# Performance work log

Hardware: AMD Instinct MI355X
Metric: run time of the kernel (lower is better)

The kernel has to match this reference:

```python
import jax, jax.numpy as jnp
import numpy as np

DIM = 512
HEADS = 8
DIM_HEAD = 64
DIM_INNER = HEADS * DIM_HEAD
FRAC_GRAD = 0.5
SCALE = DIM_HEAD ** -0.5
EPS_CUMPROD = 1e-10
EPS_INV = 1e-8


def setup_inputs() -> dict:
    key = jax.random.key(0)
    ks = jax.random.split(key, 8)
    b, n = 2, 2048
    x = jax.random.normal(ks[0], (b, n, DIM), dtype=jnp.float32)
    gamma = jnp.ones((DIM,), dtype=jnp.float32)
    w_qkv = jax.random.normal(ks[1], (DIM, 3 * DIM_INNER), dtype=jnp.float32) * 0.02
    b_qkv = jnp.zeros((3 * DIM_INNER,), dtype=jnp.float32)
    # to_a: torch init is zeros weight + bias 10; use small random weight and
    # moderate bias so the decay gate is non-trivial for correctness testing
    w_a = jax.random.normal(ks[2], (DIM, DIM_INNER), dtype=jnp.float32) * 0.02
    b_a = jnp.full((DIM_INNER,), 2.0, dtype=jnp.float32)
    w_out = jax.random.normal(ks[3], (DIM_INNER, DIM), dtype=jnp.float32) * 0.02
    b_out = jnp.zeros((DIM,), dtype=jnp.float32)
    return {"x": x, "gamma": gamma, "w_qkv": w_qkv, "b_qkv": b_qkv,
            "w_a": w_a, "b_a": b_a, "w_out": w_out, "b_out": b_out}


def _rms_norm(x, gamma):
    # F.normalize(x, dim=-1) * sqrt(dim) * gamma
    nrm = jnp.linalg.norm(x, axis=-1, keepdims=True)
    return x / jnp.maximum(nrm, 1e-12) * (DIM ** 0.5) * gamma


def _safe_cumprod(t, axis):
    t = jnp.clip(t, EPS_CUMPROD, 1.0)
    return jnp.exp(jnp.cumsum(jnp.log(t), axis=axis))


def reference(x, gamma, w_qkv, b_qkv, w_a, b_a, w_out, b_out):
    b, n, _ = x.shape
    x = _rms_norm(x, gamma)

    qkv = x @ w_qkv + b_qkv  # [b, n, 3*h*d]
    qkv = qkv.reshape(b, n, 3, HEADS, DIM_HEAD).transpose(2, 0, 3, 1, 4)  # [3,b,h,n,d]
    q, k, v = qkv[0], qkv[1], qkv[2]
    q = q * SCALE

    # data-dependent relative-position decay gate
    a = (x @ w_a + b_a).reshape(b, n, HEADS, DIM_HEAD).transpose(0, 2, 1, 3)  # [b,h,n,d]
    a = a * FRAC_GRAD + jax.lax.stop_gradient(a) * (1.0 - FRAC_GRAD)
    a = jax.nn.sigmoid(a)
    a_cum = _safe_cumprod(a, axis=-2)
    a_cum_inv = 1.0 / jnp.maximum(a_cum, EPS_INV)

    q = q * a_cum
    k = k * a_cum_inv

    sim = jnp.einsum('bhid,bhjd->bhij', q, k)
    causal_mask = jnp.triu(jnp.ones((n, n), dtype=bool), k=1)
    attn = jnp.where(causal_mask, 0.0, sim)  # no softmax in decay branch

    out = jnp.einsum('bhij,bhjd->bhid', attn, v)  # [b,h,n,d]
    out = out.transpose(0, 2, 1, 3).reshape(b, n, DIM_INNER)
    return out @ w_out + b_out
```

## Files before the change

kernel.cpp:

```cpp
#include <hip/hip_runtime.h>
#include <hip/hip_cooperative_groups.h>


namespace cg = cooperative_groups;

using s8v   = __attribute__((ext_vector_type(8))) short;
using f32x4 = __attribute__((ext_vector_type(4))) float;

__device__ __forceinline__ unsigned short f2b(float f) {
  unsigned int u = __builtin_bit_cast(unsigned int, f);
  u += 0x7FFFu + ((u >> 16) & 1u);
  return (unsigned short)(u >> 16);
}
__device__ __forceinline__ float b2f(unsigned short b) {
  unsigned int u = ((unsigned int)b) << 16;
  return __builtin_bit_cast(float, u);
}
__device__ __forceinline__ f32x4 mfma16(s8v a, s8v b, f32x4 c) {
  return __builtin_amdgcn_mfma_f32_16x16x32_bf16(a, b, c, 0, 0, 0);
}
__device__ __forceinline__ void gload16(const void* g, void* l) {
  __builtin_amdgcn_global_load_lds(
      (const __attribute__((address_space(1))) void*)g,
      (__attribute__((address_space(3))) void*)l, 16, 0, 0);
}

__device__ __forceinline__ void st_prep(int u, int tid, char* arena,
    const float* __restrict__ x, const float* __restrict__ gamma,
    short* __restrict__ xnb,
    const float* __restrict__ w_qkv, const float* __restrict__ w_a,
    const float* __restrict__ w_out,
    short* __restrict__ wT, short* __restrict__ woT) {
  int lane = tid & 63, wave = tid >> 6;
  if (u < 1024) {
    int row = u * 4 + wave;
    const float4* xp = reinterpret_cast<const float4*>(x + (size_t)row * 512 + lane * 8);
    float4 v0 = xp[0], v1 = xp[1];
    float ss = v0.x*v0.x + v0.y*v0.y + v0.z*v0.z + v0.w*v0.w
             + v1.x*v1.x + v1.y*v1.y + v1.z*v1.z + v1.w*v1.w;
#pragma unroll
    for (int off = 32; off > 0; off >>= 1) ss += __shfl_xor(ss, off, 64);
    float s = 22.627416997969522f / fmaxf(sqrtf(ss), 1e-12f);
    const float* g = gamma + lane * 8;
    float vals[8] = {v0.x, v0.y, v0.z, v0.w, v1.x, v1.y, v1.z, v1.w};
    s8v o;
#pragma unroll
    for (int j = 0; j < 8; ++j) o[j] = (short)f2b(vals[j] * s * g[j]);
    *reinterpret_cast<s8v*>(xnb + (size_t)row * 512 + lane * 8) = o;
  } else {
    float (*t)[33] = reinterpret_cast<float (*)[33]>(arena);
    int id = u - 1024;
    int bx = id % 80, k0 = (id / 80) * 32;
    const float* src; short* dst; int N, n0;
    if (bx < 48)      { src = w_qkv; dst = wT;                      N = 1536; n0 = bx * 32; }
    else if (bx < 64) { src = w_a;   dst = wT + (size_t)1536 * 512; N = 512;  n0 = (bx - 48) * 32; }
    else              { src = w_out; dst = woT;                     N = 512;  n0 = (bx - 64) * 32; }
    int tx = tid & 31, ty = tid >> 5;
    __syncthreads();
#pragma unroll
    for (int i = 0; i < 4; ++i)
      t[ty + 8 * i][tx] = src[(size_t)(k0 + ty + 8 * i) * N + n0 + tx];
    __syncthreads();
#pragma unroll
    for (int i = 0; i < 4; ++i)
      dst[(size_t)(n0 + ty + 8 * i) * 512 + k0 + tx] = (short)f2b(t[tx][ty + 8 * i]);
  }
}

template <int BM, int BN, int FM, int FN>
__device__ __forceinline__ void gemm_core(const short* __restrict__ A,
                                          const short* __restrict__ Bm,
                                          char* LA, char* LB,
                                          int m0, int n0, int tid,
                                          f32x4 (&acc)[FM][FN]) {
  const int lane = tid & 63, wave = tid >> 6;
  const int wr = (wave >> 1) * (BM / 2), wc = (wave & 1) * (BN / 2);
#pragma unroll 1
  for (int t = 0; t < 8; ++t) {
    const int k0 = t * 64;
#pragma unroll
    for (int r = 0; r < BM / 32; ++r) {
      int o = r * 4096 + tid * 16;
      int row = o >> 7;
      int ce = (((o & 127) ^ ((row & 7) << 4)) >> 1);
      gload16(A + (size_t)(m0 + row) * 512 + k0 + ce, LA + o);
    }
#pragma unroll
    for (int r = 0; r < BN / 32; ++r) {
      int o = r * 4096 + tid * 16;
      int row = o >> 7;
      int ce = (((o & 127) ^ ((row & 7) << 4)) >> 1);
      gload16(Bm + (size_t)(n0 + row) * 512 + k0 + ce, LB + o);
    }
    __syncthreads();
#pragma unroll
    for (int kk = 0; kk < 2; ++kk) {
      s8v af[FM], bf[FN];
#pragma unroll
      for (int m = 0; m < FM; ++m) {
        int row = wr + m * 16 + (lane & 15);
        int ad = ((row << 7) + kk * 64 + ((lane >> 4) << 4)) ^ ((row & 7) << 4);
        af[m] = *reinterpret_cast<const s8v*>(LA + ad);
      }
#pragma unroll
      for (int n = 0; n < FN; ++n) {
        int row = wc + n * 16 + (lane & 15);
        int ad = ((row << 7) + kk * 64 + ((lane >> 4) << 4)) ^ ((row & 7) << 4);
        bf[n] = *reinterpret_cast<const s8v*>(LB + ad);
      }
#pragma unroll
      for (int m = 0; m < FM; ++m)
#pragma unroll
        for (int n = 0; n < FN; ++n)
          acc[m][n] = mfma16(af[m], bf[n], acc[m][n]);
    }
    if (t + 1 < 8) __syncthreads();
  }
}

__device__ __forceinline__ void st_gemm0(int vid, int tid, char* arena,
    const short* __restrict__ xnb, const short* __restrict__ wT,
    short* __restrict__ qkvb, const float* __restrict__ b_qkv,
    const float* __restrict__ b_a, float* __restrict__ araw,
    float* __restrict__ csum) {
  const int lane = tid & 63, wave = tid >> 6;
  int xcd = vid & 7, rq = vid >> 3;
  int bx = rq & 15, by = xcd * 4 + (rq >> 4);
  int m0 = by * 128, n0 = bx * 128;
  f32x4 acc[4][4] = {};
  gemm_core<128, 128, 4, 4>(xnb, wT, arena, arena + 16384, m0, n0, tid, acc);
  int wr = (wave >> 1) * 64, wc = (wave & 1) * 64;
  if (n0 < 1536) {
#pragma unroll
    for (int m = 0; m < 4; ++m)
#pragma unroll
      for (int n = 0; n < 4; ++n)
#pragma unroll
        for (int r = 0; r < 4; ++r) {
          int row = m0 + wr + m * 16 + ((lane >> 4) << 2) + r;
          int col = n0 + wc + n * 16 + (lane & 15);
          float v = acc[m][n][r] + b_qkv[col];
          int w = col >> 9, h = (col >> 6) & 7, d = col & 63;
          int b = row >> 11, nn = row & 2047;
          qkvb[((((size_t)(w * 2 + b)) * 8 + h) * 2048 + nn) * 64 + d] = (short)f2b(v);
        }
  } else {
    float cs[4] = {};
    int b = m0 >> 11;
#pragma unroll
    for (int m = 0; m < 4; ++m)
#pragma unroll
      for (int n = 0; n < 4; ++n)
#pragma unroll
        for (int r = 0; r < 4; ++r) {
          int row = m0 + wr + m * 16 + ((lane >> 4) << 2) + r;
          int gc = n0 + wc + n * 16 + (lane & 15) - 1536;
          int h = gc >> 6, d = gc & 63, nn = row & 2047;
          float xv = acc[m][n][r] + b_a[gc];
          araw[((size_t)(b * 8 + h) * 2048 + nn) * 64 + d] = xv;
          float a = 1.f / (1.f + expf(-xv));
          a = fminf(fmaxf(a, 1e-10f), 1.f);
          cs[n] += logf(a);
        }
#pragma unroll
    for (int n = 0; n < 4; ++n) {
      cs[n] += __shfl_xor(cs[n], 16, 64);
      cs[n] += __shfl_xor(cs[n], 32, 64);
    }
    int nsel = lane >> 4;
    float v = (nsel == 0) ? cs[0] : (nsel == 1) ? cs[1] : (nsel == 2) ? cs[2] : cs[3];
    int col = wc + nsel * 16 + (lane & 15);
    int gc = n0 + col - 1536;
    int h = gc >> 6, d = gc & 63;
    int chunkg = ((m0 & 2047) >> 6) + (wave >> 1);
    csum[(((size_t)(b * 8 + h)) * 32 + chunkg) * 64 + d] = v;
  }
}

__device__ __forceinline__ void st_scan2(int vid, int tid, char* arena,
    const short* __restrict__ qkvb, const float* __restrict__ araw,
    const float* __restrict__ csum, short* __restrict__ q2,
    short* __restrict__ k2, short* __restrict__ vT, short* __restrict__ Sbuf) {
  int chunk = vid & 31, bh = vid >> 5;
  int lane = tid & 63, wave = tid >> 6, d = lane;
  short (*kL)[64] = reinterpret_cast<short (*)[64]>(arena);
  short (*vL)[64] = reinterpret_cast<short (*)[64]>(arena + 8192);
  char* kT  = arena + 16384;
  char* vTl = arena + 24576;
  float (*wsum)[64] = reinterpret_cast<float (*)[64]>(arena + 16384);
  float pre = 0.f;
  for (int c = 0; c < chunk; ++c) pre += csum[((size_t)bh * 32 + c) * 64 + d];
  const float* ap = araw + ((size_t)bh * 2048 + chunk * 64 + wave * 16) * 64 + d;
  float la[16]; float run = 0.f;
#pragma unroll
  for (int rr = 0; rr < 16; ++rr) {
    float xv = ap[rr * 64];
    float a = 1.f / (1.f + expf(-xv));
    a = fminf(fmaxf(a, 1e-10f), 1.f);
    run += logf(a);
    la[rr] = run;
  }
  wsum[wave][d] = run;
  __syncthreads();
#pragma unroll
  for (int w = 0; w < 3; ++w) if (w < wave) pre += wsum[w][d];
  const size_t WS = (size_t)2 * 8 * 2048 * 64;
  size_t base = ((size_t)bh * 2048 + chunk * 64 + wave * 16) * 64 + d;
#pragma unroll 4
  for (int rr = 0; rr < 16; ++rr) {
    int r = wave * 16 + rr;
    float g = expf(pre + la[rr]);
    float gi = 1.f / fmaxf(g, 1e-8f);
    float qv = b2f((unsigned short)qkvb[base + rr * 64]);
    float kv = b2f((unsigned short)qkvb[base + WS + rr * 64]);
    short vb = qkvb[base + 2 * WS + rr * 64];
    q2[base + rr * 64] = (short)f2b(qv * 0.125f * g);
    unsigned short kb = f2b(kv * gi);
    k2[base + rr * 64] = (short)kb;
    kL[r][d] = (short)kb;
    vL[r][d] = vb;
  }
  __syncthreads();
  short* vTrow = vT + ((size_t)bh * 64 + d) * 2048 + chunk * 64;
#pragma unroll
  for (int gg = 0; gg < 2; ++gg) {
    int g8 = wave + gg * 4;
    s8v pk, pv;
#pragma unroll
    for (int j = 0; j < 8; ++j) { pk[j] = kL[g8 * 8 + j][d]; pv[j] = vL[g8 * 8 + j][d]; }
    *reinterpret_cast<s8v*>(vTrow + g8 * 8) = pv;
    int ad = ((d << 7) + g8 * 16) ^ ((d & 7) << 4);
    *reinterpret_cast<s8v*>(kT  + ad) = pk;
    *reinterpret_cast<s8v*>(vTl + ad) = pv;
  }
  __syncthreads();
  f32x4 acc[4] = {};
#pragma unroll
  for (int kk = 0; kk < 2; ++kk) {
    int arow = wave * 16 + (lane & 15);
    int aad = ((arow << 7) + kk * 64 + ((lane >> 4) << 4)) ^ ((arow & 7) << 4);
    s8v av = *reinterpret_cast<const s8v*>(vTl + aad);
#pragma unroll
    for (int n = 0; n < 4; ++n) {
      int brow = n * 16 + (lane & 15);
      int bad = ((brow << 7) + kk * 64 + ((lane >> 4) << 4)) ^ ((brow & 7) << 4);
      acc[n] = mfma16(av, *reinterpret_cast<const s8v*>(kT + bad), acc[n]);
    }
  }
  short* Sp = Sbuf + ((size_t)bh * 32 + chunk) * 4096;
#pragma unroll
  for (int n = 0; n < 4; ++n)
#pragma unroll
    for (int r = 0; r < 4; ++r)
      Sp[(wave * 16 + ((lane >> 4) << 2) + r) * 64 + n * 16 + (lane & 15)] = (short)f2b(acc[n][r]);
}

__device__ __forceinline__ void st_sprefix(int vid, int tid,
    const short* __restrict__ Sbuf, short* __restrict__ Spre) {
  int bh = vid >> 4;
  int e = ((vid & 15) << 8) + tid;
  size_t base = (size_t)bh * 32 * 4096 + e;
  float acc = 0.f;
  for (int c = 0; c < 32; ++c) {
    Spre[base + (size_t)c * 4096] = (short)f2b(acc);
    acc += b2f((unsigned short)Sbuf[base + (size_t)c * 4096]);
  }
}

__device__ __forceinline__ void st_attnk(int vid, int tid, char* arena,
    const short* __restrict__ q2, const short* __restrict__ k2,
    const short* __restrict__ vT, const short* __restrict__ Spre,
    short* __restrict__ aout) {
  int chunk = vid & 31, bh = vid >> 5;
  int lane = tid & 63, wave = tid >> 6;
  char* LQ = arena;
  char* LK = arena + 8192;
  char* LV = arena + 16384;
  char* LS = arena + 24576;
#pragma unroll
  for (int rr = 0; rr < 2; ++rr) {
    int o = rr * 4096 + tid * 16;
    int row = o >> 7;
    int ce = (((o & 127) ^ ((row & 7) << 4)) >> 1);
    gload16(q2   + ((size_t)bh * 2048 + chunk * 64 + row) * 64 + ce, LQ + o);
    gload16(k2   + ((size_t)bh * 2048 + chunk * 64 + row) * 64 + ce, LK + o);
    gload16(vT   + ((size_t)bh * 64 + row) * 2048 + chunk * 64 + ce, LV + o);
    gload16(Spre + (((size_t)bh * 32 + chunk) * 64 + row) * 64 + ce, LS + o);
  }
  __syncthreads();
  f32x4 accS[4] = {}, accO[4] = {};
#pragma unroll
  for (int kk = 0; kk < 2; ++kk) {
    int arow = wave * 16 + (lane & 15);
    int aad = ((arow << 7) + kk * 64 + ((lane >> 4) << 4)) ^ ((arow & 7) << 4);
    s8v aq = *reinterpret_cast<const s8v*>(LQ + aad);
#pragma unroll
    for (int n = 0; n < 4; ++n) {
      int brow = n * 16 + (lane & 15);
      int bad = ((brow << 7) + kk * 64 + ((lane >> 4) << 4)) ^ ((brow & 7) << 4);
      accS[n] = mfma16(aq, *reinterpret_cast<const s8v*>(LK + bad), accS[n]);
      accO[n] = mfma16(aq, *reinterpret_cast<const s8v*>(LS + bad), accO[n]);
    }
  }
  __syncthreads();
#pragma unroll
  for (int n = 0; n < 4; ++n)
#pragma unroll
    for (int r = 0; r < 4; ++r) {
      int i = wave * 16 + ((lane >> 4) << 2) + r;
      int j = n * 16 + (lane & 15);
      float v = (j <= i) ? accS[n][r] : 0.f;
      int ad = ((i << 7) + (j << 1)) ^ ((i & 7) << 4);
      *reinterpret_cast<short*>(LQ + ad) = (short)f2b(v);
    }
  __syncthreads();
#pragma unroll
  for (int kk = 0; kk < 2; ++kk) {
    int arow = wave * 16 + (lane & 15);
    int aad = ((arow << 7) + kk * 64 + ((lane >> 4) << 4)) ^ ((arow & 7) << 4);
    s8v ap = *reinterpret_cast<const s8v*>(LQ + aad);
#pragma unroll
    for (int n = 0; n < 4; ++n) {
      int brow = n * 16 + (lane & 15);
      int bad = ((brow << 7) + kk * 64 + ((lane >> 4) << 4)) ^ ((brow & 7) << 4);
      accO[n] = mfma16(ap, *reinterpret_cast<const s8v*>(LV + bad), accO[n]);
    }
  }
  int b = bh >> 3, h = bh & 7;
#pragma unroll
  for (int n = 0; n < 4; ++n)
#pragma unroll
    for (int r = 0; r < 4; ++r) {
      int i = wave * 16 + ((lane >> 4) << 2) + r;
      int col = h * 64 + n * 16 + (lane & 15);
      size_t row = (size_t)b * 2048 + chunk * 64 + i;
      aout[row * 512 + col] = (short)f2b(accO[n][r]);
    }
}

__device__ __forceinline__ void st_gemm1(int vid, int tid, char* arena,
    const short* __restrict__ aout, const short* __restrict__ woT,
    float* __restrict__ out, const float* __restrict__ b_out) {
  const int lane = tid & 63, wave = tid >> 6;
  int xcd = vid & 7, rq = vid >> 3;
  int bx = rq & 7, by = xcd * 8 + (rq >> 3);
  int m0 = by * 64, n0 = bx * 64;
  f32x4 acc[2][2] = {};
  gemm_core<64, 64, 2, 2>(aout, woT, arena, arena + 8192, m0, n0, tid, acc);
  int wr = (wave >> 1) * 32, wc = (wave & 1) * 32;
#pragma unroll
  for (int m = 0; m < 2; ++m)
#pragma unroll
    for (int n = 0; n < 2; ++n)
#pragma unroll
      for (int r = 0; r < 4; ++r) {
        int row = m0 + wr + m * 16 + ((lane >> 4) << 2) + r;
        int col = n0 + wc + n * 16 + (lane & 15);
        out[(size_t)row * 512 + col] = acc[m][n][r] + b_out[col];
      }
}

__global__ __launch_bounds__(256, 2) void mega_k(
    const float* __restrict__ x, const float* __restrict__ gamma,
    const float* __restrict__ w_qkv, const float* __restrict__ b_qkv,
    const float* __restrict__ w_a, const float* __restrict__ b_a,
    const float* __restrict__ w_out, const float* __restrict__ b_out,
    float* __restrict__ out,
    short* __restrict__ xnb, short* __restrict__ wT, short* __restrict__ woT,
    short* __restrict__ qkvb, float* __restrict__ araw, float* __restrict__ csum,
    short* __restrict__ q2, short* __restrict__ k2, short* __restrict__ vT,
    short* __restrict__ Sbuf, short* __restrict__ Spre, short* __restrict__ aout) {
  __shared__ __align__(16) char arena[32768];
  cg::grid_group grid = cg::this_grid();
  const int bid = blockIdx.x, tid = threadIdx.x;

  for (int u = bid; u < 2304; u += 512)
    st_prep(u, tid, arena, x, gamma, xnb, w_qkv, w_a, w_out, wT, woT);
  __threadfence(); grid.sync();

  st_gemm0(bid, tid, arena, xnb, wT, qkvb, b_qkv, b_a, araw, csum);
  __threadfence(); grid.sync();

  st_scan2(bid, tid, arena, qkvb, araw, csum, q2, k2, vT, Sbuf);
  __threadfence(); grid.sync();

  if (bid < 256) st_sprefix(bid, tid, Sbuf, Spre);
  __threadfence(); grid.sync();

  st_attnk(bid, tid, arena, q2, k2, vT, Spre, aout);
  __threadfence(); grid.sync();

  st_gemm1(bid, tid, arena, aout, woT, out, b_out);
}

__global__ __launch_bounds__(256) void prep_k(const float* x, const float* gamma,
    short* xnb, const float* w_qkv, const float* w_a, const float* w_out,
    short* wT, short* woT) {
  __shared__ __align__(16) char arena[4224];
  st_prep(blockIdx.x, threadIdx.x, arena, x, gamma, xnb, w_qkv, w_a, w_out, wT, woT);
}
__global__ __launch_bounds__(256) void gemm0_k(const short* xnb, const short* wT,
    short* qkvb, const float* b_qkv, const float* b_a, float* araw, float* csum) {
  __shared__ __align__(16) char arena[32768];
  st_gemm0(blockIdx.x, threadIdx.x, arena, xnb, wT, qkvb, b_qkv, b_a, araw, csum);
}
__global__ __launch_bounds__(256) void scan2_k(const short* qkvb, const float* araw,
    const float* csum, short* q2, short* k2, short* vT, short* Sbuf) {
  __shared__ __align__(16) char arena[32768];
  st_scan2(blockIdx.x, threadIdx.x, arena, qkvb, araw, csum, q2, k2, vT, Sbuf);
}
__global__ __launch_bounds__(256) void sprefix_k(const short* Sbuf, short* Spre) {
  st_sprefix(blockIdx.x, threadIdx.x, Sbuf, Spre);
}
__global__ __launch_bounds__(256) void attnk_k(const short* q2, const short* k2,
    const short* vT, const short* Spre, short* aout) {
  __shared__ __align__(16) char arena[32768];
  st_attnk(blockIdx.x, threadIdx.x, arena, q2, k2, vT, Spre, aout);
}
__global__ __launch_bounds__(256) void gemm1_k(const short* aout, const short* woT,
    float* out, const float* b_out) {
  __shared__ __align__(16) char arena[16384];
  st_gemm1(blockIdx.x, threadIdx.x, arena, aout, woT, out, b_out);
}

extern "C" void kernel_launch(void* const* d_in, const int* in_sizes, int n_in,
                              void* d_out, int out_size, void* d_ws, size_t ws_size,
                              hipStream_t stream) {
  const float* x     = (const float*)d_in[0];
  const float* gamma = (const float*)d_in[1];
  const float* w_qkv = (const float*)d_in[2];
  const float* b_qkv = (const float*)d_in[3];
  const float* w_a   = (const float*)d_in[4];
  const float* b_a   = (const float*)d_in[5];
  const float* w_out = (const float*)d_in[6];
  const float* b_out = (const float*)d_in[7];
  float* out = (float*)d_out;
  char* ws = (char*)d_ws;

  const size_t MB = 1u << 20;
  short* xnb  = (short*)(ws);
  short* wT   = (short*)(ws + 4  * MB);
  short* woT  = (short*)(ws + 6  * MB);
  short* qkvb = (short*)(ws + 7  * MB);
  float* araw = (float*)(ws + 19 * MB);
  float* csum = (float*)(ws + 27 * MB);
  short* q2   = (short*)(ws + 28 * MB);
  short* k2   = (short*)(ws + 32 * MB);
  short* vT   = (short*)(ws + 36 * MB);
  short* Sbuf = (short*)(ws + 40 * MB);
  short* Spre = (short*)(ws + 44 * MB);
  short* aout = (short*)(ws + 48 * MB);

  int dev = 0; (void)hipGetDevice(&dev);
  int coop = 0;
  (void)hipDeviceGetAttribute(&coop, hipDeviceAttributeCooperativeLaunch, dev);
  int nb = 0;
  (void)hipOccupancyMaxActiveBlocksPerMultiprocessor(&nb, mega_k, 256, 0);

  hipError_t err = hipErrorUnknown;
  if (coop && nb >= 2) {
    void* args[] = {&x, &gamma, &w_qkv, &b_qkv, &w_a, &b_a, &w_out, &b_out,
                    &out, &xnb, &wT, &woT, &qkvb, &araw, &csum,
                    &q2, &k2, &vT, &Sbuf, &Spre, &aout};
    err = hipLaunchCooperativeKernel((void*)mega_k, dim3(512), dim3(256), args, 0, stream);
  }
  if (err != hipSuccess) {
    prep_k   <<<2304, 256, 0, stream>>>(x, gamma, xnb, w_qkv, w_a, w_out, wT, woT);
    gemm0_k  <<<512,  256, 0, stream>>>(xnb, wT, qkvb, b_qkv, b_a, araw, csum);
    scan2_k  <<<512,  256, 0, stream>>>(qkvb, araw, csum, q2, k2, vT, Sbuf);
    sprefix_k<<<256,  256, 0, stream>>>(Sbuf, Spre);
    attnk_k  <<<512,  256, 0, stream>>>(q2, k2, vT, Spre, aout);
    gemm1_k  <<<512,  256, 0, stream>>>(aout, woT, out, b_out);
  }
}
```

Baseline: 70.98 us.

## Keep q/k/v chunk tiles in LDS across grid syncs in cooperative megakernel

```diff
diff --git a/kernel.cpp b/kernel.cpp
--- a/kernel.cpp
+++ b/kernel.cpp
@@ -368,11 +368,11 @@
     float* __restrict__ out,
     short* __restrict__ xnb, short* __restrict__ wT, short* __restrict__ woT,
     short* __restrict__ qkvb, float* __restrict__ araw, float* __restrict__ csum,
-    short* __restrict__ q2, short* __restrict__ k2, short* __restrict__ vT,
     short* __restrict__ Sbuf, short* __restrict__ Spre, short* __restrict__ aout) {
   __shared__ __align__(16) char arena[32768];
   cg::grid_group grid = cg::this_grid();
   const int bid = blockIdx.x, tid = threadIdx.x;
+  const int lane = tid & 63, wave = tid >> 6;
 
   for (int u = bid; u < 2304; u += 512)
     st_prep(u, tid, arena, x, gamma, xnb, w_qkv, w_a, w_out, wT, woT);
@@ -381,13 +381,147 @@
   st_gemm0(bid, tid, arena, xnb, wT, qkvb, b_qkv, b_a, araw, csum);
   __threadfence(); grid.sync();
 
-  st_scan2(bid, tid, arena, qkvb, araw, csum, q2, k2, vT, Sbuf);
+  const int chunk = bid & 31, bh = bid >> 5;
+  const int d = lane;
+  char* qL  = arena;
+  char* kR  = arena + 8192;
+  char* kT  = arena + 16384;
+  char* vTl = arena + 24576;
+  f32x4 accO[4] = {};
+  {
+    float (*wsum)[64] = reinterpret_cast<float (*)[64]>(kR);
+    float pre = 0.f;
+    for (int c = 0; c < chunk; ++c) pre += csum[((size_t)bh * 32 + c) * 64 + d];
+    const float* ap = araw + ((size_t)bh * 2048 + chunk * 64 + wave * 16) * 64 + d;
+    float la[16]; float run = 0.f;
+#pragma unroll
+    for (int rr = 0; rr < 16; ++rr) {
+      float xv = ap[rr * 64];
+      float a = 1.f / (1.f + expf(-xv));
+      a = fminf(fmaxf(a, 1e-10f), 1.f);
+      run += logf(a);
+      la[rr] = run;
+    }
+    wsum[wave][d] = run;
+    __syncthreads();
+#pragma unroll
+    for (int w = 0; w < 3; ++w) if (w < wave) pre += wsum[w][d];
+    __syncthreads();
+    const size_t WS = (size_t)2 * 8 * 2048 * 64;
+    size_t base = ((size_t)bh * 2048 + chunk * 64 + wave * 16) * 64 + d;
+#pragma unroll 4
+    for (int rr = 0; rr < 16; ++rr) {
+      int r = wave * 16 + rr;
+      float g = expf(pre + la[rr]);
+      float gi = 1.f / fmaxf(g, 1e-8f);
+      float qv = b2f((unsigned short)qkvb[base + rr * 64]);
+      float kv = b2f((unsigned short)qkvb[base + WS + rr * 64]);
+      short vb = qkvb[base + 2 * WS + rr * 64];
+      unsigned short qb = f2b(qv * 0.125f * g);
+      unsigned short kb = f2b(kv * gi);
+      int adr = ((r << 7) + (d << 1)) ^ ((r & 7) << 4);
+      *reinterpret_cast<short*>(qL + adr) = (short)qb;
+      *reinterpret_cast<short*>(kR + adr) = (short)kb;
+      int adt = ((d << 7) + (r << 1)) ^ ((d & 7) << 4);
+      *reinterpret_cast<short*>(kT  + adt) = (short)kb;
+      *reinterpret_cast<short*>(vTl + adt) = vb;
+    }
+    __syncthreads();
+    f32x4 sacc[4] = {};
+#pragma unroll
+    for (int kk = 0; kk < 2; ++kk) {
+      int arow = wave * 16 + (lane & 15);
+      int aad = ((arow << 7) + kk * 64 + ((lane >> 4) << 4)) ^ ((arow & 7) << 4);
+      s8v av = *reinterpret_cast<const s8v*>(vTl + aad);
+#pragma unroll
+      for (int n = 0; n < 4; ++n) {
+        int brow = n * 16 + (lane & 15);
+        int bad = ((brow << 7) + kk * 64 + ((lane >> 4) << 4)) ^ ((brow & 7) << 4);
+        sacc[n] = mfma16(av, *reinterpret_cast<const s8v*>(kT + bad), sacc[n]);
+      }
+    }
+    short* Sp = Sbuf + ((size_t)bh * 32 + chunk) * 4096;
+#pragma unroll
+    for (int n = 0; n < 4; ++n)
+#pragma unroll
+      for (int r = 0; r < 4; ++r)
+        Sp[(wave * 16 + ((lane >> 4) << 2) + r) * 64 + n * 16 + (lane & 15)] = (short)f2b(sacc[n][r]);
+    f32x4 accS[4] = {};
+#pragma unroll
+    for (int kk = 0; kk < 2; ++kk) {
+      int arow = wave * 16 + (lane & 15);
+      int aad = ((arow << 7) + kk * 64 + ((lane >> 4) << 4)) ^ ((arow & 7) << 4);
+      s8v aq = *reinterpret_cast<const s8v*>(qL + aad);
+#pragma unroll
+      for (int n = 0; n < 4; ++n) {
+        int brow = n * 16 + (lane & 15);
+        int bad = ((brow << 7) + kk * 64 + ((lane >> 4) << 4)) ^ ((brow & 7) << 4);
+        accS[n] = mfma16(aq, *reinterpret_cast<const s8v*>(kR + bad), accS[n]);
+      }
+    }
+    __syncthreads();
+#pragma unroll
+    for (int n = 0; n < 4; ++n)
+#pragma unroll
+      for (int r = 0; r < 4; ++r) {
+        int i = wave * 16 + ((lane >> 4) << 2) + r;
+        int j = n * 16 + (lane & 15);
+        float v = (j <= i) ? accS[n][r] : 0.f;
+        int ad = ((i << 7) + (j << 1)) ^ ((i & 7) << 4);
+        *reinterpret_cast<short*>(kT + ad) = (short)f2b(v);
+      }
+    __syncthreads();
+#pragma unroll
+    for (int kk = 0; kk < 2; ++kk) {
+      int arow = wave * 16 + (lane & 15);
+      int aad = ((arow << 7) + kk * 64 + ((lane >> 4) << 4)) ^ ((arow & 7) << 4);
+      s8v ap = *reinterpret_cast<const s8v*>(kT + aad);
+#pragma unroll
+      for (int n = 0; n < 4; ++n) {
+        int brow = n * 16 + (lane & 15);
+        int bad = ((brow << 7) + kk * 64 + ((lane >> 4) << 4)) ^ ((brow & 7) << 4);
+        accO[n] = mfma16(ap, *reinterpret_cast<const s8v*>(vTl + bad), accO[n]);
+      }
+    }
+  }
   __threadfence(); grid.sync();
 
   if (bid < 256) st_sprefix(bid, tid, Sbuf, Spre);
   __threadfence(); grid.sync();
 
-  st_attnk(bid, tid, arena, q2, k2, vT, Spre, aout);
+  {
+    char* LS = kR;
+#pragma unroll
+    for (int rr = 0; rr < 2; ++rr) {
+      int o = rr * 4096 + tid * 16;
+      int row = o >> 7;
+      int ce = (((o & 127) ^ ((row & 7) << 4)) >> 1);
+      gload16(Spre + (((size_t)bh * 32 + chunk) * 64 + row) * 64 + ce, LS + o);
+    }
+    __syncthreads();
+#pragma unroll
+    for (int kk = 0; kk < 2; ++kk) {
+      int arow = wave * 16 + (lane & 15);
+      int aad = ((arow << 7) + kk * 64 + ((lane >> 4) << 4)) ^ ((arow & 7) << 4);
+      s8v aq = *reinterpret_cast<const s8v*>(qL + aad);
+#pragma unroll
+      for (int n = 0; n < 4; ++n) {
+        int brow = n * 16 + (lane & 15);
+        int bad = ((brow << 7) + kk * 64 + ((lane >> 4) << 4)) ^ ((brow & 7) << 4);
+        accO[n] = mfma16(aq, *reinterpret_cast<const s8v*>(LS + bad), accO[n]);
+      }
+    }
+    int b = bh >> 3, h = bh & 7;
+#pragma unroll
+    for (int n = 0; n < 4; ++n)
+#pragma unroll
+      for (int r = 0; r < 4; ++r) {
+        int i = wave * 16 + ((lane >> 4) << 2) + r;
+        int col = h * 64 + n * 16 + (lane & 15);
+        size_t row = (size_t)b * 2048 + chunk * 64 + i;
+        aout[row * 512 + col] = (short)f2b(accO[n][r]);
+      }
+  }
   __threadfence(); grid.sync();
 
   st_gemm1(bid, tid, arena, aout, woT, out, b_out);
@@ -444,12 +578,12 @@
   short* qkvb = (short*)(ws + 7  * MB);
   float* araw = (float*)(ws + 19 * MB);
   float* csum = (float*)(ws + 27 * MB);
-  short* q2   = (short*)(ws + 28 * MB);
-  short* k2   = (short*)(ws + 32 * MB);
-  short* vT   = (short*)(ws + 36 * MB);
-  short* Sbuf = (short*)(ws + 40 * MB);
-  short* Spre = (short*)(ws + 44 * MB);
-  short* aout = (short*)(ws + 48 * MB);
+  short* Sbuf = (short*)(ws + 28 * MB);
+  short* Spre = (short*)(ws + 32 * MB);
+  short* aout = (short*)(ws + 36 * MB);
+  short* q2   = (short*)(ws + 40 * MB);
+  short* k2   = (short*)(ws + 44 * MB);
+  short* vT   = (short*)(ws + 48 * MB);
 
   int dev = 0; (void)hipGetDevice(&dev);
   int coop = 0;
@@ -461,7 +595,7 @@
   if (coop && nb >= 2) {
     void* args[] = {&x, &gamma, &w_qkv, &b_qkv, &w_a, &b_a, &w_out, &b_out,
                     &out, &xnb, &wT, &woT, &qkvb, &araw, &csum,
-                    &q2, &k2, &vT, &Sbuf, &Spre, &aout};
+                    &Sbuf, &Spre, &aout};
     err = hipLaunchCooperativeKernel((void*)mega_k, dim3(512), dim3(256), args, 0, stream);
   }
   if (err != hipSuccess) {
```

New measurement: 70.96 us. No clear change (-0.0%).
